# Kernel tuning notes

Hardware: AMD Instinct MI355X
Metric: run time of the kernel (lower is better)

Reference implementation:

```python
import jax, jax.numpy as jnp
import numpy as np
import math

NUM_BUCKETS = 32
MAX_DISTANCE = 128
N_HEADS = 16
D_KV = 64


def _relative_position_bucket(relative_position, num_buckets=NUM_BUCKETS, max_distance=MAX_DISTANCE):
    # bidirectional (encoder) variant: is_decoder=False
    nb = num_buckets // 2
    rel_buckets = (relative_position > 0).astype(jnp.int32) * nb
    rp = jnp.abs(relative_position)
    max_exact = nb // 2
    is_small = rp < max_exact
    rp_large = max_exact + (
        jnp.log(rp.astype(jnp.float32) / max_exact)
        / math.log(max_distance / max_exact)
        * (nb - max_exact)
    ).astype(jnp.int32)
    rp_large = jnp.minimum(rp_large, nb - 1)
    return rel_buckets + jnp.where(is_small, rp, rp_large)


def compute_position_bias(rel_bias_table, q_len, k_len):
    ctx = jnp.arange(q_len, dtype=jnp.int32)[:, None]
    mem = jnp.arange(k_len, dtype=jnp.int32)[None, :]
    buckets = _relative_position_bucket(mem - ctx)  # [q_len, k_len]
    values = rel_bias_table[buckets]                # [q_len, k_len, H]
    return jnp.transpose(values, (2, 0, 1))[None]   # [1, H, q_len, k_len]


def setup_inputs() -> dict:
    key = jax.random.key(0)
    ks = jax.random.split(key, 6)
    B, S, D = 2, 2048, 1024
    s = 0.02
    return {
        "hidden_states": jax.random.normal(ks[0], (B, S, D), dtype=jnp.float32),
        "Wq": jax.random.normal(ks[1], (D, N_HEADS * D_KV), dtype=jnp.float32) * s,
        "Wk": jax.random.normal(ks[2], (D, N_HEADS * D_KV), dtype=jnp.float32) * s,
        "Wv": jax.random.normal(ks[3], (D, N_HEADS * D_KV), dtype=jnp.float32) * s,
        "Wo": jax.random.normal(ks[4], (N_HEADS * D_KV, D), dtype=jnp.float32) * s,
        "rel_bias_table": jax.random.normal(ks[5], (NUM_BUCKETS, N_HEADS), dtype=jnp.float32),
    }


def reference(hidden_states, Wq, Wk, Wv, Wo, rel_bias_table):
    B, S, D = hidden_states.shape
    H, dh = N_HEADS, D_KV
    q = (hidden_states @ Wq).reshape(B, S, H, dh)
    k = (hidden_states @ Wk).reshape(B, S, H, dh)
    v = (hidden_states @ Wv).reshape(B, S, H, dh)

    position_bias = compute_position_bias(rel_bias_table, S, S)  # [1,H,S,S]

    scale = 1.0 / math.sqrt(dh)  # applied inside optimized_attention (SDPA convention)
    scores = jnp.einsum('bqhd,bkhd->bhqk', q, k) * scale + position_bias
    probs = jax.nn.softmax(scores, axis=-1)
    ctx = jnp.einsum('bhqk,bkhd->bqhd', probs, v).reshape(B, S, H * dh)
    attn_output = ctx @ Wo
    return attn_output
```

## Files before the change

kernel.cpp:

```cpp
#include <hip/hip_runtime.h>

typedef __attribute__((ext_vector_type(8))) short s16x8;
typedef __attribute__((ext_vector_type(4))) short s16x4;
typedef __attribute__((ext_vector_type(4))) float f32x4;
typedef __attribute__((ext_vector_type(4))) unsigned int u32x4;
typedef __attribute__((ext_vector_type(2))) unsigned int u32x2;
typedef unsigned short u16;
typedef unsigned int u32;

#define LOG2E 1.4426950408889634f

__device__ __forceinline__ u16 f2bf(float x) {
  u32 u = __float_as_uint(x);
  u += 0x7FFFu + ((u >> 16) & 1u);
  return (u16)(u >> 16);
}

__device__ __forceinline__ float bf2f(u16 x) {
  return __uint_as_float((u32)x << 16);
}

__device__ __forceinline__ u32 pack_bf_trunc(float lo, float hi) {
  return __builtin_amdgcn_perm(__float_as_uint(hi), __float_as_uint(lo), 0x07060302u);
}

__device__ __forceinline__ void gl_lds16(const void* g, void* l) {
  __builtin_amdgcn_global_load_lds((const __attribute__((address_space(1))) void*)g,
                                   (__attribute__((address_space(3))) void*)l, 16, 0, 0);
}

#define MFMA16(a, b, c) __builtin_amdgcn_mfma_f32_16x16x32_bf16((a), (b), (c), 0, 0, 0)


__global__ __launch_bounds__(256) void prep(const float* __restrict__ hs,
                                            const float* __restrict__ Wq,
                                            const float* __restrict__ Wk,
                                            const float* __restrict__ Wv,
                                            const float* __restrict__ Wo,
                                            const float* __restrict__ tbl,
                                            u16* __restrict__ hsb,
                                            u16* __restrict__ wt,
                                            u16* __restrict__ wot,
                                            float* __restrict__ biasT) {
  const int blk = blockIdx.x;
  const int tid = threadIdx.x;
  if (blk < 2048) {
    const int i = blk * 256 + tid;
    const float4* s4 = (const float4*)hs;
    float4 a = s4[i * 2];
    float4 b = s4[i * 2 + 1];
    s16x8 o;
    o[0] = (short)f2bf(a.x); o[1] = (short)f2bf(a.y);
    o[2] = (short)f2bf(a.z); o[3] = (short)f2bf(a.w);
    o[4] = (short)f2bf(b.x); o[5] = (short)f2bf(b.y);
    o[6] = (short)f2bf(b.z); o[7] = (short)f2bf(b.w);
    *(s16x8*)&hsb[i * 8] = o;
  } else if (blk < 4096) {
    int r = blk - 2048;
    const int sel = r >> 9;
    r &= 511;
    const float* W = sel == 0 ? Wq : (sel == 1 ? Wk : (sel == 2 ? Wv : Wo));
    u16* dst = sel == 3 ? wot : wt + sel * 1048576;
    const int n = (r & 15) * 64 + (tid & 63);
    const int kb = (r >> 4) * 32 + (tid >> 6) * 8;
    s16x8 o;
#pragma unroll
    for (int j = 0; j < 8; ++j) o[j] = (short)f2bf(W[(kb + j) * 1024 + n]);
    *(s16x8*)&dst[n * 1024 + kb] = o;
  } else {
    const int i = (blk - 4096) * 256 + tid;
    const int h = i >> 12, dp = i & 4095;
    const int delta = dp - 2047;
    const int rp = delta < 0 ? -delta : delta;
    int bucket = delta > 0 ? 16 : 0;
    if (rp < 8)
      bucket += rp;
    else
      bucket += 8 + (rp >= 12) + (rp >= 16) + (rp >= 23) + (rp >= 32) +
                (rp >= 46) + (rp >= 64) + (rp >= 91);
    biasT[i] = tbl[bucket * 16 + h] * LOG2E;
  }
}


__device__ __forceinline__ void gemm_core(const u16* __restrict__ A,
                                          const u16* __restrict__ Bt,
                                          int m0, int n0,
                                          u16* shbuf, f32x4 acc[4][4]) {
  const int tid = threadIdx.x;
  const int w = tid >> 6, l = tid & 63, g = l >> 4, m15 = l & 15;
  const int wr = (w >> 1) * 64, wc = (w & 1) * 64;
#pragma unroll
  for (int i = 0; i < 4; ++i)
#pragma unroll
    for (int j = 0; j < 4; ++j) acc[i][j] = (f32x4){0.f, 0.f, 0.f, 0.f};

#define GSTAGE(buf, k0)                                                    \
  {                                                                        \
    _Pragma("unroll") for (int c = 0; c < 2; ++c) {                        \
      const int idx = c * 256 + tid;                                       \
      const int row = idx >> 2, col4 = idx & 3;                            \
      const int scol = col4 ^ ((row >> 1) & 3);                            \
      gl_lds16(&A[(m0 + row) * 1024 + (k0) + scol * 8],                    \
               (char*)shbuf + (buf)*8192 + c * 4096 + w * 1024);           \
      gl_lds16(&Bt[(n0 + row) * 1024 + (k0) + scol * 8],                   \
               (char*)shbuf + 16384 + (buf)*8192 + c * 4096 + w * 1024);   \
    }                                                                      \
  }

  GSTAGE(0, 0);
  int cur = 0;
  for (int kt = 0; kt < 32; ++kt) {
    __syncthreads();
    if (kt < 31) GSTAGE(cur ^ 1, (kt + 1) * 32);
    const u16* Asb = shbuf + cur * 4096;
    const u16* Bsb = shbuf + 8192 + cur * 4096;
    s16x8 af[4], bfr[4];
#pragma unroll
    for (int mf = 0; mf < 4; ++mf) {
      const int row = wr + mf * 16 + m15;
      af[mf] = *(const s16x8*)&Asb[(row * 4 + (g ^ ((row >> 1) & 3))) * 8];
    }
#pragma unroll
    for (int nf = 0; nf < 4; ++nf) {
      const int row = wc + nf * 16 + m15;
      bfr[nf] = *(const s16x8*)&Bsb[(row * 4 + (g ^ ((row >> 1) & 3))) * 8];
    }
#pragma unroll
    for (int mf = 0; mf < 4; ++mf)
#pragma unroll
      for (int nf = 0; nf < 4; ++nf)
        acc[mf][nf] = MFMA16(af[mf], bfr[nf], acc[mf][nf]);
    cur ^= 1;
  }
#undef GSTAGE
}

__global__ __launch_bounds__(256) void gemm_qkv(const u16* __restrict__ X,
                                                const u16* __restrict__ Wt,
                                                u16* __restrict__ Q,
                                                u16* __restrict__ Kb,
                                                u16* __restrict__ VT) {
  __shared__ u16 shbuf[16384];
  f32x4 acc[4][4];
  const int flat = blockIdx.x;
  const int x = flat & 7, i = flat >> 3;
  const int m0 = ((x & 3) * 8 + (i & 7)) * 128;
  const int n0 = ((x >> 2) * 12 + (i >> 3)) * 128;
  gemm_core(X, Wt, m0, n0, shbuf, acc);

  const int tid = threadIdx.x;
  const int w = tid >> 6, l = tid & 63, g = l >> 4, m15 = l & 15;
  const int wr = (w >> 1) * 64, wc = (w & 1) * 64;
  const int nsel = n0 >> 10;
  const int ncol0 = (n0 & 1023) + wc;
  if (nsel == 2) {
    __syncthreads();
#pragma unroll
    for (int mf = 0; mf < 4; ++mf) {
      const int s_base = wr + mf * 16 + g * 4;
#pragma unroll
      for (int nf = 0; nf < 4; ++nf) {
        const int d_loc = wc + nf * 16 + m15;
        s16x4 pk;
#pragma unroll
        for (int r = 0; r < 4; ++r) pk[r] = (short)f2bf(acc[mf][nf][r]);
        *(s16x4*)&shbuf[d_loc * 128 + (s_base ^ ((d_loc & 7) << 3))] = pk;
      }
    }
    __syncthreads();
    const int b = m0 >> 11, sg0 = m0 & 2047;
#pragma unroll
    for (int it = 0; it < 8; ++it) {
      const int d_loc = it * 16 + w * 4 + g;
      const s16x8 v =
          *(const s16x8*)&shbuf[d_loc * 128 + ((m15 * 8) ^ ((d_loc & 7) << 3))];
      const int col = (n0 & 1023) + d_loc;
      *(s16x8*)&VT[((b * 16 + (col >> 6)) * 64 + (col & 63)) * 2048 + sg0 + m15 * 8] = v;
    }
  } else {
    u16* dst = nsel == 0 ? Q : Kb;
    const float scale = nsel == 0 ? 0.125f * LOG2E : 1.0f;
#pragma unroll
    for (int mf = 0; mf < 4; ++mf) {
      const int rbase = m0 + wr + mf * 16 + g * 4;
#pragma unroll
      for (int nf = 0; nf < 4; ++nf) {
        const int col = ncol0 + nf * 16 + m15;
#pragma unroll
        for (int r = 0; r < 4; ++r)
          dst[(rbase + r) * 1024 + col] = f2bf(acc[mf][nf][r] * scale);
      }
    }
  }
}

__global__ __launch_bounds__(256) void gemm_out(const u16* __restrict__ CTX,
                                                const u16* __restrict__ Wot,
                                                float* __restrict__ Out) {
  __shared__ u16 shbuf[16384];
  f32x4 acc[4][4];
  const int flat = blockIdx.x;
  const int x = flat & 7, i = flat >> 3;
  const int m0 = ((x & 3) * 8 + (i & 7)) * 128;
  const int n0 = ((x >> 2) * 4 + (i >> 3)) * 128;
  gemm_core(CTX, Wot, m0, n0, shbuf, acc);

  const int tid = threadIdx.x;
  const int w = tid >> 6, l = tid & 63, g = l >> 4, m15 = l & 15;
  const int wr = (w >> 1) * 64, wc = (w & 1) * 64;
#pragma unroll
  for (int mf = 0; mf < 4; ++mf) {
    const int rbase = m0 + wr + mf * 16 + g * 4;
#pragma unroll
    for (int nf = 0; nf < 4; ++nf) {
      const int col = n0 + wc + nf * 16 + m15;
#pragma unroll
      for (int r = 0; r < 4; ++r)
        Out[(rbase + r) * 1024 + col] = acc[mf][nf][r];
    }
  }
}


__global__ __launch_bounds__(256, 4) void attn_kernel(const u16* __restrict__ Qg,
                                                      const u16* __restrict__ Kg,
                                                      const u16* __restrict__ VTg,
                                                      const float* __restrict__ biasT,
                                                      const float* __restrict__ tbl,
                                                      u16* __restrict__ po0,
                                                      u16* __restrict__ po1,
                                                      u16* __restrict__ po2,
                                                      u16* __restrict__ po3,
                                                      float* __restrict__ pls) {
  __shared__ u16 KT[2][4096];
  __shared__ u16 VTs[2][4096];

  const int tid = threadIdx.x;
  const int w = tid >> 6, l = tid & 63, g = l >> 4, m15 = l & 15;
  const int flat = blockIdx.x;
  const int nf_ = (flat & 7) * 256 + (flat >> 3);
  const int bh = nf_ >> 6;
  const int rem = nf_ & 63;
  const int quarter = rem >> 4, qblk = rem & 15;
  const int b = bh >> 4, h = bh & 15;
  const int qw = qblk * 128 + w * 32;
  const int kvbase = quarter * 512;

  u16* poh = quarter == 0 ? po0 : (quarter == 1 ? po1 : (quarter == 2 ? po2 : po3));
  float* plsh = pls + quarter * 65536;

  const float fpos = tbl[31 * 16 + h] * LOG2E;
  const float fneg = tbl[15 * 16 + h] * LOG2E;

  s16x8 aq[2][2];
#pragma unroll
  for (int qs = 0; qs < 2; ++qs) {
    const u16* qp = &Qg[(b * 2048 + qw + qs * 16 + m15) * 1024 + h * 64 + g * 8];
    aq[qs][0] = *(const s16x8*)qp;
    aq[qs][1] = *(const s16x8*)(qp + 32);
  }

  s16x8 vone;
#pragma unroll
  for (int j = 0; j < 8; ++j) vone[j] = (short)0x3F80;

  f32x4 o[2][4];
  f32x4 ls4[2];
#pragma unroll
  for (int qs = 0; qs < 2; ++qs) {
    ls4[qs] = (f32x4){0.f, 0.f, 0.f, 0.f};
#pragma unroll
    for (int d = 0; d < 4; ++d) o[qs][d] = (f32x4){0.f, 0.f, 0.f, 0.f};
  }

  const u16* Kbase = &Kg[(b * 2048 + kvbase) * 1024 + h * 64];
  const u16* Vbase = &VTg[bh * 64 * 2048 + kvbase];

#define STAGE(buf, kv0)                                                          \
  {                                                                              \
    _Pragma("unroll") for (int c = 0; c < 2; ++c) {                              \
      const int idx = c * 256 + tid;                                             \
      const int row = idx >> 3, col16 = idx & 7;                                 \
      const int scol = col16 ^ (row & 7);                                        \
      gl_lds16(&Kbase[(kv0 + row) * 1024 + scol * 8],                            \
               (char*)KT + (buf)*8192 + c * 4096 + w * 1024);                    \
      gl_lds16(&Vbase[row * 2048 + (kv0) + scol * 8],                            \
               (char*)VTs + (buf)*8192 + c * 4096 + w * 1024);                   \
    }                                                                            \
  }

  STAGE(0, 0);
  int cur = 0;
  for (int t = 0; t < 8; ++t) {
    const int kv0 = t * 64;
    __syncthreads();
    if (t < 7) STAGE(cur ^ 1, kv0 + 64);

    const u16* KTc = &KT[cur][0];
    const u16* VTc = &VTs[cur][0];

    f32x4 s[2][4];
    const int diff = kvbase + kv0 - qw;
    if (diff <= -160 || diff >= 128) {
      const float bc = diff > 0 ? fpos : fneg;
#pragma unroll
      for (int qs = 0; qs < 2; ++qs)
#pragma unroll
        for (int c = 0; c < 4; ++c) s[qs][c] = (f32x4){bc, bc, bc, bc};
    } else {
#pragma unroll
      for (int qs = 0; qs < 2; ++qs) {
        const float* bp =
            &biasT[h * 4096 + kvbase + kv0 + g * 4 - qw - qs * 16 - m15 + 2047];
#pragma unroll
        for (int c = 0; c < 4; ++c)
#pragma unroll
          for (int r = 0; r < 4; ++r) s[qs][c][r] = bp[c * 16 + r];
      }
    }

    __builtin_amdgcn_s_setprio(1);
#pragma unroll
    for (int ks = 0; ks < 2; ++ks) {
#pragma unroll
      for (int c = 0; c < 4; ++c) {
        const int row = c * 16 + m15;
        const s16x8 bk = *(const s16x8*)&KTc[(row * 8 + ((ks * 4 + g) ^ (row & 7))) * 8];
        s[0][c] = MFMA16(bk, aq[0][ks], s[0][c]);
        s[1][c] = MFMA16(bk, aq[1][ks], s[1][c]);
      }
    }
    __builtin_amdgcn_s_setprio(0);

    s16x8 pa[2][2];
#pragma unroll
    for (int qs = 0; qs < 2; ++qs) {
      u32 w01[4], w23[4];
#pragma unroll
      for (int c = 0; c < 4; ++c) {
        w01[c] = pack_bf_trunc(__builtin_amdgcn_exp2f(s[qs][c][0]),
                               __builtin_amdgcn_exp2f(s[qs][c][1]));
        w23[c] = pack_bf_trunc(__builtin_amdgcn_exp2f(s[qs][c][2]),
                               __builtin_amdgcn_exp2f(s[qs][c][3]));
      }
#pragma unroll
      for (int ks = 0; ks < 2; ++ks) {
        u32x2 rA = __builtin_amdgcn_permlane32_swap(w01[2 * ks], w01[2 * ks + 1], false, false);
        u32x2 rB = __builtin_amdgcn_permlane16_swap(rA[0], rA[1], false, false);
        u32x2 rC = __builtin_amdgcn_permlane32_swap(w23[2 * ks], w23[2 * ks + 1], false, false);
        u32x2 rD = __builtin_amdgcn_permlane16_swap(rC[0], rC[1], false, false);
        const u32x4 pd = (u32x4){rB[0], rD[0], rB[1], rD[1]};
        pa[qs][ks] = __builtin_bit_cast(s16x8, pd);
      }
    }

    __builtin_amdgcn_s_setprio(1);
#pragma unroll
    for (int ks = 0; ks < 2; ++ks) {
#pragma unroll
      for (int d = 0; d < 4; ++d) {
        const int rowv = d * 16 + m15;
        const s16x8 bv = *(const s16x8*)&VTc[(rowv * 8 + ((ks * 4 + g) ^ (rowv & 7))) * 8];
        o[0][d] = MFMA16(pa[0][ks], bv, o[0][d]);
        o[1][d] = MFMA16(pa[1][ks], bv, o[1][d]);
      }
      ls4[0] = MFMA16(pa[0][ks], vone, ls4[0]);
      ls4[1] = MFMA16(pa[1][ks], vone, ls4[1]);
    }
    __builtin_amdgcn_s_setprio(0);
    cur ^= 1;
  }
#undef STAGE

#pragma unroll
  for (int qs = 0; qs < 2; ++qs) {
    const int orow = b * 2048 + qw + qs * 16 + g * 4;
    const int ocol = h * 64 + m15;
#pragma unroll
    for (int r = 0; r < 4; ++r) {
#pragma unroll
      for (int d = 0; d < 4; ++d)
        poh[(orow + r) * 1024 + ocol + d * 16] = f2bf(o[qs][d][r]);
      if (m15 == 0) plsh[(orow + r) * 16 + h] = ls4[qs][r];
    }
  }
}

__global__ __launch_bounds__(256) void merge(const u16* po0, const u16* po1,
                                             const u16* po2, const u16* po3,
                                             const float* pls, u16* outp) {
  const int i = blockIdx.x * 256 + threadIdx.x;
  const int row = i >> 7;
  const int seg = i & 127;
  const int h = seg >> 3;
  const int li = row * 16 + h;
  const float den =
      1.0f / (pls[li] + pls[65536 + li] + pls[131072 + li] + pls[196608 + li]);
  const int base = row * 1024 + seg * 8;
  const s16x8 a = *(const s16x8*)&po0[base];
  const s16x8 b = *(const s16x8*)&po1[base];
  const s16x8 c = *(const s16x8*)&po2[base];
  const s16x8 d = *(const s16x8*)&po3[base];
  s16x8 o;
#pragma unroll
  for (int j = 0; j < 8; ++j)
    o[j] = (short)f2bf((bf2f((u16)a[j]) + bf2f((u16)b[j]) +
                        bf2f((u16)c[j]) + bf2f((u16)d[j])) * den);
  *(s16x8*)&outp[base] = o;
}


extern "C" void kernel_launch(void* const* d_in, const int* in_sizes, int n_in,
                              void* d_out, int out_size, void* d_ws, size_t ws_size,
                              hipStream_t stream) {
  (void)in_sizes; (void)n_in; (void)out_size; (void)ws_size;
  const float* hs  = (const float*)d_in[0];
  const float* Wq  = (const float*)d_in[1];
  const float* Wk  = (const float*)d_in[2];
  const float* Wv  = (const float*)d_in[3];
  const float* Wo  = (const float*)d_in[4];
  const float* tbl = (const float*)d_in[5];

  char* ws = (char*)d_ws;
  u16* hsb   = (u16*)(ws);
  u16* wt    = (u16*)(ws + 8388608);
  u16* wot   = (u16*)(ws + 14680064);
  u16* q     = (u16*)(ws + 16777216);
  u16* k     = (u16*)(ws + 25165824);
  u16* po0   = (u16*)(ws + 33554432);
  u16* vt    = (u16*)(ws + 41943040);
  u16* po2   = (u16*)(ws + 50331648);
  float* biasT = (float*)(ws + 58720256);
  u16* po1   = hsb;
  u16* po3   = (u16*)d_out;
  float* pls = (float*)wt;

  prep<<<4352, 256, 0, stream>>>(hs, Wq, Wk, Wv, Wo, tbl, hsb, wt, wot, biasT);
  gemm_qkv<<<768, 256, 0, stream>>>(hsb, wt, q, k, vt);
  attn_kernel<<<2048, 256, 0, stream>>>(q, k, vt, biasT, tbl, po0, po1, po2, po3, pls);
  merge<<<2048, 256, 0, stream>>>(po0, po1, po2, po3, pls, po0);
  gemm_out<<<256, 256, 0, stream>>>(po0, wot, (float*)d_out);
}
```

Measured before the change: 123.0 us.

## Store K and V in MFMA fragment layout and load directly into registers

```diff
diff --git a/kernel.cpp b/kernel.cpp
--- a/kernel.cpp
+++ b/kernel.cpp
@@ -139,8 +139,8 @@
 __global__ __launch_bounds__(256) void gemm_qkv(const u16* __restrict__ X,
                                                 const u16* __restrict__ Wt,
                                                 u16* __restrict__ Q,
-                                                u16* __restrict__ Kb,
-                                                u16* __restrict__ VT) {
+                                                u16* __restrict__ KF,
+                                                u16* __restrict__ VF) {
   __shared__ u16 shbuf[16384];
   f32x4 acc[4][4];
   const int flat = blockIdx.x;
@@ -153,34 +153,9 @@
   const int w = tid >> 6, l = tid & 63, g = l >> 4, m15 = l & 15;
   const int wr = (w >> 1) * 64, wc = (w & 1) * 64;
   const int nsel = n0 >> 10;
-  const int ncol0 = (n0 & 1023) + wc;
-  if (nsel == 2) {
-    __syncthreads();
-#pragma unroll
-    for (int mf = 0; mf < 4; ++mf) {
-      const int s_base = wr + mf * 16 + g * 4;
-#pragma unroll
-      for (int nf = 0; nf < 4; ++nf) {
-        const int d_loc = wc + nf * 16 + m15;
-        s16x4 pk;
-#pragma unroll
-        for (int r = 0; r < 4; ++r) pk[r] = (short)f2bf(acc[mf][nf][r]);
-        *(s16x4*)&shbuf[d_loc * 128 + (s_base ^ ((d_loc & 7) << 3))] = pk;
-      }
-    }
-    __syncthreads();
-    const int b = m0 >> 11, sg0 = m0 & 2047;
-#pragma unroll
-    for (int it = 0; it < 8; ++it) {
-      const int d_loc = it * 16 + w * 4 + g;
-      const s16x8 v =
-          *(const s16x8*)&shbuf[d_loc * 128 + ((m15 * 8) ^ ((d_loc & 7) << 3))];
-      const int col = (n0 & 1023) + d_loc;
-      *(s16x8*)&VT[((b * 16 + (col >> 6)) * 64 + (col & 63)) * 2048 + sg0 + m15 * 8] = v;
-    }
-  } else {
-    u16* dst = nsel == 0 ? Q : Kb;
-    const float scale = nsel == 0 ? 0.125f * LOG2E : 1.0f;
+  if (nsel == 0) {
+    const float scale = 0.125f * LOG2E;
+    const int ncol0 = (n0 & 1023) + wc;
 #pragma unroll
     for (int mf = 0; mf < 4; ++mf) {
       const int rbase = m0 + wr + mf * 16 + g * 4;
@@ -189,8 +164,65 @@
         const int col = ncol0 + nf * 16 + m15;
 #pragma unroll
         for (int r = 0; r < 4; ++r)
-          dst[(rbase + r) * 1024 + col] = f2bf(acc[mf][nf][r] * scale);
-      }
+          Q[(rbase + r) * 1024 + col] = f2bf(acc[mf][nf][r] * scale);
+      }
+    }
+  } else {
+    __syncthreads();
+    if (nsel == 1) {
+#pragma unroll
+      for (int mf = 0; mf < 4; ++mf) {
+        const int s_base = wr + mf * 16 + g * 4;
+#pragma unroll
+        for (int nf = 0; nf < 4; ++nf) {
+          const int d_loc = wc + nf * 16 + m15;
+          const int dc = d_loc >> 3, db = d_loc & 7;
+#pragma unroll
+          for (int r = 0; r < 4; ++r) {
+            const int s = s_base + r;
+            shbuf[s * 128 + (dc ^ (s & 7)) * 8 + db] = f2bf(acc[mf][nf][r]);
+          }
+        }
+      }
+    } else {
+#pragma unroll
+      for (int mf = 0; mf < 4; ++mf) {
+        const int s_base = wr + mf * 16 + g * 4;
+#pragma unroll
+        for (int nf = 0; nf < 4; ++nf) {
+          const int d_loc = wc + nf * 16 + m15;
+          s16x4 pk;
+#pragma unroll
+          for (int r = 0; r < 4; ++r) pk[r] = (short)f2bf(acc[mf][nf][r]);
+          *(s16x4*)&shbuf[d_loc * 128 + (s_base ^ ((d_loc & 7) << 3))] = pk;
+        }
+      }
+    }
+    __syncthreads();
+    u16* dstF = nsel == 1 ? KF : VF;
+    const int b = m0 >> 11;
+    const int hbase = (n0 & 1023) >> 6;
+    const int tbase = (m0 & 2047) >> 6;
+#pragma unroll
+    for (int it = 0; it < 8; ++it) {
+      const int fid = it * 256 + tid;
+      const int lslot = fid & 63;
+      const int word = fid >> 6;
+      const int cc = word & 3, ks = (word >> 2) & 1;
+      const int h_l = (word >> 3) & 1, t_l = word >> 4;
+      const int m15s = lslot & 15, gs = lslot >> 4;
+      s16x8 v;
+      if (nsel == 1) {
+        const int s_loc = t_l * 64 + cc * 16 + m15s;
+        const int D0 = h_l * 64 + ks * 32 + gs * 8;
+        v = *(const s16x8*)&shbuf[s_loc * 128 + ((D0 >> 3) ^ (s_loc & 7)) * 8];
+      } else {
+        const int d_loc = h_l * 64 + cc * 16 + m15s;
+        const int S0 = t_l * 64 + ks * 32 + gs * 8;
+        v = *(const s16x8*)&shbuf[d_loc * 128 + (S0 ^ ((d_loc & 7) << 3))];
+      }
+      *(s16x8*)&dstF[((b * 16 + hbase + h_l) * 32 + tbase + t_l) * 4096 +
+                     (ks * 4 + cc) * 512 + lslot * 8] = v;
     }
   }
 }
@@ -224,8 +256,8 @@
 
 
 __global__ __launch_bounds__(256, 4) void attn_kernel(const u16* __restrict__ Qg,
-                                                      const u16* __restrict__ Kg,
-                                                      const u16* __restrict__ VTg,
+                                                      const u16* __restrict__ KF,
+                                                      const u16* __restrict__ VF,
                                                       const float* __restrict__ biasT,
                                                       const float* __restrict__ tbl,
                                                       u16* __restrict__ po0,
@@ -233,9 +265,6 @@
                                                       u16* __restrict__ po2,
                                                       u16* __restrict__ po3,
                                                       float* __restrict__ pls) {
-  __shared__ u16 KT[2][4096];
-  __shared__ u16 VTs[2][4096];
-
   const int tid = threadIdx.x;
   const int w = tid >> 6, l = tid & 63, g = l >> 4, m15 = l & 15;
   const int flat = blockIdx.x;
@@ -274,31 +303,13 @@
     for (int d = 0; d < 4; ++d) o[qs][d] = (f32x4){0.f, 0.f, 0.f, 0.f};
   }
 
-  const u16* Kbase = &Kg[(b * 2048 + kvbase) * 1024 + h * 64];
-  const u16* Vbase = &VTg[bh * 64 * 2048 + kvbase];
-
-#define STAGE(buf, kv0)                                                          \
-  {                                                                              \
-    _Pragma("unroll") for (int c = 0; c < 2; ++c) {                              \
-      const int idx = c * 256 + tid;                                             \
-      const int row = idx >> 3, col16 = idx & 7;                                 \
-      const int scol = col16 ^ (row & 7);                                        \
-      gl_lds16(&Kbase[(kv0 + row) * 1024 + scol * 8],                            \
-               (char*)KT + (buf)*8192 + c * 4096 + w * 1024);                    \
-      gl_lds16(&Vbase[row * 2048 + (kv0) + scol * 8],                            \
-               (char*)VTs + (buf)*8192 + c * 4096 + w * 1024);                   \
-    }                                                                            \
-  }
-
-  STAGE(0, 0);
-  int cur = 0;
+  const u16* KFb = KF + (bh * 32 + quarter * 8) * 4096 + l * 8;
+  const u16* VFb = VF + (bh * 32 + quarter * 8) * 4096 + l * 8;
+
   for (int t = 0; t < 8; ++t) {
     const int kv0 = t * 64;
-    __syncthreads();
-    if (t < 7) STAGE(cur ^ 1, kv0 + 64);
-
-    const u16* KTc = &KT[cur][0];
-    const u16* VTc = &VTs[cur][0];
+    const u16* KFt = KFb + t * 4096;
+    const u16* VFt = VFb + t * 4096;
 
     f32x4 s[2][4];
     const int diff = kvbase + kv0 - qw;
@@ -320,18 +331,30 @@
       }
     }
 
+    s16x8 bk[2][4];
+#pragma unroll
+    for (int ks = 0; ks < 2; ++ks)
+#pragma unroll
+      for (int c = 0; c < 4; ++c)
+        bk[ks][c] = *(const s16x8*)&KFt[(ks * 4 + c) * 512];
+
     __builtin_amdgcn_s_setprio(1);
 #pragma unroll
     for (int ks = 0; ks < 2; ++ks) {
 #pragma unroll
       for (int c = 0; c < 4; ++c) {
-        const int row = c * 16 + m15;
-        const s16x8 bk = *(const s16x8*)&KTc[(row * 8 + ((ks * 4 + g) ^ (row & 7))) * 8];
-        s[0][c] = MFMA16(bk, aq[0][ks], s[0][c]);
-        s[1][c] = MFMA16(bk, aq[1][ks], s[1][c]);
+        s[0][c] = MFMA16(bk[ks][c], aq[0][ks], s[0][c]);
+        s[1][c] = MFMA16(bk[ks][c], aq[1][ks], s[1][c]);
       }
     }
     __builtin_amdgcn_s_setprio(0);
+
+    s16x8 bv[2][4];
+#pragma unroll
+    for (int ks = 0; ks < 2; ++ks)
+#pragma unroll
+      for (int d = 0; d < 4; ++d)
+        bv[ks][d] = *(const s16x8*)&VFt[(ks * 4 + d) * 512];
 
     s16x8 pa[2][2];
 #pragma unroll
@@ -360,18 +383,14 @@
     for (int ks = 0; ks < 2; ++ks) {
 #pragma unroll
       for (int d = 0; d < 4; ++d) {
-        const int rowv = d * 16 + m15;
-        const s16x8 bv = *(const s16x8*)&VTc[(rowv * 8 + ((ks * 4 + g) ^ (rowv & 7))) * 8];
-        o[0][d] = MFMA16(pa[0][ks], bv, o[0][d]);
-        o[1][d] = MFMA16(pa[1][ks], bv, o[1][d]);
+        o[0][d] = MFMA16(pa[0][ks], bv[ks][d], o[0][d]);
+        o[1][d] = MFMA16(pa[1][ks], bv[ks][d], o[1][d]);
       }
       ls4[0] = MFMA16(pa[0][ks], vone, ls4[0]);
       ls4[1] = MFMA16(pa[1][ks], vone, ls4[1]);
     }
     __builtin_amdgcn_s_setprio(0);
-    cur ^= 1;
-  }
-#undef STAGE
+  }
 
 #pragma unroll
   for (int qs = 0; qs < 2; ++qs) {
@@ -427,9 +446,9 @@
   u16* wt    = (u16*)(ws + 8388608);
   u16* wot   = (u16*)(ws + 14680064);
   u16* q     = (u16*)(ws + 16777216);
-  u16* k     = (u16*)(ws + 25165824);
+  u16* kf    = (u16*)(ws + 25165824);
   u16* po0   = (u16*)(ws + 33554432);
-  u16* vt    = (u16*)(ws + 41943040);
+  u16* vf    = (u16*)(ws + 41943040);
   u16* po2   = (u16*)(ws + 50331648);
   float* biasT = (float*)(ws + 58720256);
   u16* po1   = hsb;
@@ -437,8 +456,8 @@
   float* pls = (float*)wt;
 
   prep<<<4352, 256, 0, stream>>>(hs, Wq, Wk, Wv, Wo, tbl, hsb, wt, wot, biasT);
-  gemm_qkv<<<768, 256, 0, stream>>>(hsb, wt, q, k, vt);
-  attn_kernel<<<2048, 256, 0, stream>>>(q, k, vt, biasT, tbl, po0, po1, po2, po3, pls);
+  gemm_qkv<<<768, 256, 0, stream>>>(hsb, wt, q, kf, vf);
+  attn_kernel<<<2048, 256, 0, stream>>>(q, kf, vf, biasT, tbl, po0, po1, po2, po3, pls);
   merge<<<2048, 256, 0, stream>>>(po0, po1, po2, po3, pls, po0);
   gemm_out<<<256, 256, 0, stream>>>(po0, wot, (float*)d_out);
 }
```

After: 134.0 us. 9.0% more time.
